# Optimization experiments

Hardware: AMD Instinct MI355X
Metric: run time of the kernel (lower is better)

Reference implementation:

```python
import jax, jax.numpy as jnp
import numpy as np

H, F, K, R = 8, 64, 10, 256  # num_heads, in_features, num_sines, num_realizations
B, L = 4, 2048


def setup_inputs() -> dict:
    key = jax.random.key(0)
    k1, k2, k3, k4, k5, k6 = jax.random.split(key, 6)
    return {
        "queries": jax.random.normal(k1, (B, L, H, F), dtype=jnp.float32),
        "keys": jax.random.normal(k2, (B, L, H, F), dtype=jnp.float32),
        "z": jax.random.normal(k3, (B, H, F, 2 * K, R), dtype=jnp.float32),
        "freqs": jax.random.normal(k4, (H, F, K), dtype=jnp.float32),
        "offsets": jax.random.normal(k5, (H, F, K), dtype=jnp.float32),
        "gains": jax.random.normal(k6, (H, F, K), dtype=jnp.float32),
    }


def reference(queries, keys, z, freqs, offsets, gains):
    h, f_dim, k_sines = freqs.shape
    length = queries.shape[1]
    r = z.shape[-1]
    # split positional / non-positional features (rest is empty here: key_dim == in_features)
    q_pos, q_rest = queries[..., :f_dim], queries[..., f_dim:]
    k_pos, k_rest = keys[..., :f_dim], keys[..., f_dim:]

    idx = jnp.arange(length, dtype=queries.dtype)  # linspace(0, L-1, L)
    fr = jax.nn.sigmoid(freqs)[:, :, None, :] / 2.0          # [H, F, 1, K]
    base = 2.0 * jnp.pi * fr * idx[None, None, :, None]       # [H, F, L, K]
    ph_q = base + offsets[:, :, None, :]
    ph_k = base
    # stack(cos, sin) on last axis then flatten -> interleaved cos0,sin0,... : [H, F, L, 2K]
    omega_q = jnp.stack([jnp.cos(ph_q), jnp.sin(ph_q)], axis=-1).reshape(h, f_dim, length, 2 * k_sines)
    omega_k = jnp.stack([jnp.cos(ph_k), jnp.sin(ph_k)], axis=-1).reshape(h, f_dim, length, 2 * k_sines)

    g = jnp.tile(jax.nn.softplus(gains), (1, 1, 2))           # [H, F, 2K] (block-repeated, as in torch .repeat)
    zs = z * g[None, :, :, :, None] / np.sqrt(r * f_dim).astype(np.float32)  # [B, H, F, 2K, R]

    # fused double contraction over f (in_features) and s (2K sines); equals
    # (omega @ z) permuted then multiplied by queries and summed over in_features
    qhat = jnp.einsum('hfls,bhfsr,blhf->blhr', omega_q, zs, q_pos)  # [B, L, H, R]
    khat = jnp.einsum('hfls,bhfsr,blhf->blhr', omega_k, zs, k_pos)

    qhat = jnp.concatenate([qhat, q_rest], axis=-1)
    khat = jnp.concatenate([khat, k_rest], axis=-1)
    return qhat, khat
```

## Files before the change

### kernel.cpp

```cpp
#include <hip/hip_runtime.h>
#include <math.h>


#define NH 8
#define NF 64
#define NK 10
#define NR 256
#define NB 4
#define NL 2048
#define KTOT 1280
#define BM 128
#define BK 32
#define NCH (KTOT/BK)
#define NFRAG_B 16
#define WS_NEEDED ((size_t)NB*NH*NCH*NFRAG_B*1024)

typedef __attribute__((ext_vector_type(8))) short short8;
typedef __attribute__((ext_vector_type(4))) float f32x4;
typedef __attribute__((ext_vector_type(4))) unsigned int u32x4;

static __device__ __forceinline__ unsigned short f2b(float f) {
    unsigned x = __float_as_uint(f);
    return (unsigned short)((x + 0x7FFFu + ((x >> 16) & 1u)) >> 16);
}
static __device__ __forceinline__ unsigned int pk2(float a, float b) {
    return (unsigned int)f2b(a) | ((unsigned int)f2b(b) << 16);
}
static __device__ __forceinline__ void gload_lds16(const void* g, void* l) {
    __builtin_amdgcn_global_load_lds(
        (const __attribute__((address_space(1))) unsigned int*)g,
        (__attribute__((address_space(3))) unsigned int*)l, 16, 0, 0);
}

__global__ __launch_bounds__(256)
void spe_prep(const float* __restrict__ z, const float* __restrict__ gains,
              unsigned char* __restrict__ bpack)
{
    __shared__ float s_g[NF*NK];
    const int ch  = blockIdx.x;
    const int bh  = blockIdx.y;
    const int h   = bh & 7;
    const int tid = threadIdx.x;
    for (int i = tid; i < NF*NK; i += 256)
        s_g[i] = log1pf(expf(gains[h*NF*NK + i])) * 0.0078125f;
    __syncthreads();
    const float* zb = z + (size_t)bh * KTOT * NR;
    unsigned char* dst = bpack + ((size_t)(bh*NCH + ch) * NFRAG_B) * 1024;
    #pragma unroll
    for (int it = 0; it < 4; ++it) {
        const int s  = tid + 256*it;
        const int fi = s >> 6;
        const int l  = s & 63;
        const int r  = fi*16 + (l & 15);
        const int k0 = ch*BK + (l >> 4)*8;
        u32x4 wv;
        #pragma unroll
        for (int jp = 0; jp < 4; ++jp) {
            const int ka = k0 + 2*jp, kb = ka + 1;
            const int fa = (ka*3277) >> 16; int sa = ka - fa*20; if (sa >= NK) sa -= NK;
            const int fb = (kb*3277) >> 16; int sb = kb - fb*20; if (sb >= NK) sb -= NK;
            const float va = zb[(size_t)ka*NR + r] * s_g[fa*NK + sa];
            const float vb = zb[(size_t)kb*NR + r] * s_g[fb*NK + sb];
            wv[jp] = pk2(va, vb);
        }
        *(u32x4*)(dst + (size_t)s*16) = wv;
    }
}

#define OFF_B0  0
#define OFF_B1  16384
#define OFF_A   32768
#define OFF_POS 40960
#define OFF_FR  57472
#define OFF_OF  60032
#define SMEM_SZ 62592

__global__ __launch_bounds__(512, 4)
void spe_main(const float* __restrict__ queries, const float* __restrict__ keys,
              const float* __restrict__ freqs, const float* __restrict__ offsets,
              const unsigned char* __restrict__ bpack, float* __restrict__ out)
{
    __shared__ __attribute__((aligned(16))) unsigned char smem[SMEM_SZ];
    const int tid  = threadIdx.x;
    const int lane = tid & 63;
    const int w    = tid >> 6;
    const int l0   = blockIdx.x * BM;
    const int bh   = blockIdx.y;
    const int b = bh >> 3, h = bh & 7;
    const int isK  = blockIdx.z;

    float* ld_fr = (float*)(smem + OFF_FR);
    float* ld_of = (float*)(smem + OFF_OF);
    unsigned short* pos_t = (unsigned short*)(smem + OFF_POS);

    for (int i = tid; i < NF*NK; i += 512) {
        const float fv = freqs[h*NF*NK + i];
        ld_fr[i] = 0.5f / (1.0f + expf(-fv));
        ld_of[i] = isK ? 0.0f : offsets[h*NF*NK + i] * 0.15915494309189535f;
    }
    {
        const float* pos = isK ? keys : queries;
        #pragma unroll
        for (int i = 0; i < 4; ++i) {
            const int lrow = (tid >> 4) + 32*i;
            const int f0   = (tid & 15) * 4;
            const float4 v = *(const float4*)(pos + ((size_t)((b*NL + l0 + lrow)*NH + h))*NF + f0);
            pos_t[(f0+0)*129 + lrow] = f2b(v.x);
            pos_t[(f0+1)*129 + lrow] = f2b(v.y);
            pos_t[(f0+2)*129 + lrow] = f2b(v.z);
            pos_t[(f0+3)*129 + lrow] = f2b(v.w);
        }
    }
    __syncthreads();

    const unsigned char* bp = bpack + (size_t)bh * ((size_t)NCH*NFRAG_B*1024);
    const int fi0 = w*2;
    gload_lds16(bp + (size_t)fi0*1024 + lane*16,       smem + OFF_B0 + (fi0  <<10));
    gload_lds16(bp + (size_t)(fi0+1)*1024 + lane*16,   smem + OFF_B0 + ((fi0+1)<<10));

    const int wm = w >> 2, wn = w & 3;
    f32x4 acc[4][4];
    #pragma unroll
    for (int mi = 0; mi < 4; ++mi)
        #pragma unroll
        for (int ni = 0; ni < 4; ++ni)
            acc[mi][ni] = (f32x4){0.f, 0.f, 0.f, 0.f};

    const int o_m = tid & 3;
    const int m_m = tid >> 2;
    const float lf = (float)(l0 + m_m);
    const int a_byte = (m_m >> 4)*1024 + (o_m*16 + (m_m & 15))*16;

    for (int t = 0; t < NCH; ++t) {
        unsigned char* Bcur = smem + ((t & 1) ? OFF_B1 : OFF_B0);
        unsigned char* Bnxt = smem + ((t & 1) ? OFF_B0 : OFF_B1);

        u32x4 wv;
        #pragma unroll
        for (int jp = 0; jp < 4; ++jp) {
            const int kk   = t*BK + o_m*8 + 2*jp;
            const int f    = (kk*3277) >> 16;
            const int srem = kk - f*20;
            const int kidx = f*NK + (srem >> 1);
            const float x  = __builtin_amdgcn_fractf(ld_of[kidx] + ld_fr[kidx]*lf);
            const float c  = __builtin_amdgcn_cosf(x);
            const float sn = __builtin_amdgcn_sinf(x);
            const float p  = __uint_as_float(((unsigned)pos_t[f*129 + m_m]) << 16);
            wv[jp] = pk2(c*p, sn*p);
        }

        asm volatile("s_waitcnt vmcnt(0)" ::: "memory");
        __builtin_amdgcn_sched_barrier(0);
        __builtin_amdgcn_s_barrier();

        if (t + 1 < NCH) {
            gload_lds16(bp + (size_t)((t+1)*NFRAG_B + fi0)*1024 + lane*16,
                        Bnxt + (fi0<<10));
            gload_lds16(bp + (size_t)((t+1)*NFRAG_B + fi0+1)*1024 + lane*16,
                        Bnxt + ((fi0+1)<<10));
        }

        *(u32x4*)(smem + OFF_A + a_byte) = wv;
        asm volatile("s_waitcnt lgkmcnt(0)" ::: "memory");
        __builtin_amdgcn_sched_barrier(0);
        __builtin_amdgcn_s_barrier();

        short8 bf[4];
        #pragma unroll
        for (int ni = 0; ni < 4; ++ni)
            bf[ni] = *(const short8*)(Bcur + ((wn*4 + ni) << 10) + (lane << 4));
        #pragma unroll
        for (int mi = 0; mi < 4; ++mi) {
            const short8 af = *(const short8*)(smem + OFF_A + ((wm*4 + mi) << 10) + (lane << 4));
            #pragma unroll
            for (int ni = 0; ni < 4; ++ni)
                acc[mi][ni] = __builtin_amdgcn_mfma_f32_16x16x32_bf16(af, bf[ni], acc[mi][ni], 0, 0, 0);
        }
    }

    const size_t qk_off = (size_t)isK * ((size_t)NB*NL*NH*NR);
    const int row_l = (lane >> 4) * 4;
    const int col_r = lane & 15;
    #pragma unroll
    for (int mi = 0; mi < 4; ++mi) {
        const int lg = l0 + wm*64 + mi*16 + row_l;
        #pragma unroll
        for (int ni = 0; ni < 4; ++ni) {
            const int rg = wn*64 + ni*16 + col_r;
            const f32x4 v = acc[mi][ni];
            #pragma unroll
            for (int q = 0; q < 4; ++q)
                out[qk_off + ((size_t)((b*NL + lg + q)*NH + h))*NR + rg] = v[q];
        }
    }
}

#define FOFF_B   0
#define FOFF_A   32768
#define FOFF_POS 49152
#define FOFF_FR  65536
#define FOFF_OFS 68096
#define FOFF_GS  70656
#define FSMEM_SZ 73216

__global__ __launch_bounds__(512, 4)
void spe_mfma_fb(const float* __restrict__ queries, const float* __restrict__ keys,
                 const float* __restrict__ z, const float* __restrict__ freqs,
                 const float* __restrict__ offsets, const float* __restrict__ gains,
                 float* __restrict__ out)
{
    __shared__ __attribute__((aligned(16))) unsigned char smem[FSMEM_SZ];
    const int tid = threadIdx.x, lane = tid & 63;
    const int l0 = blockIdx.x * BM, bh = blockIdx.y;
    const int b = bh >> 3, h = bh & 7, isK = blockIdx.z;
    float* ld_fr = (float*)(smem + FOFF_FR);
    float* ld_of = (float*)(smem + FOFF_OFS);
    float* ld_gs = (float*)(smem + FOFF_GS);
    unsigned short* pos_t = (unsigned short*)(smem + FOFF_POS);
    for (int i = tid; i < NF*NK; i += 512) {
        const float fv = freqs[h*NF*NK + i];
        ld_fr[i] = 0.5f / (1.0f + expf(-fv));
        ld_of[i] = isK ? 0.0f : offsets[h*NF*NK + i] * 0.15915494309189535f;
        ld_gs[i] = log1pf(expf(gains[h*NF*NK + i])) * 0.0078125f;
    }
    {
        const float* pos = isK ? keys : queries;
        #pragma unroll
        for (int i = 0; i < 4; ++i) {
            const int lrow = (tid >> 4) + 32*i;
            const int f0 = (tid & 15) * 4;
            const float4 v = *(const float4*)(pos + ((size_t)((b*NL + l0 + lrow)*NH + h))*NF + f0);
            pos_t[(f0+0)*BM + lrow] = f2b(v.x); pos_t[(f0+1)*BM + lrow] = f2b(v.y);
            pos_t[(f0+2)*BM + lrow] = f2b(v.z); pos_t[(f0+3)*BM + lrow] = f2b(v.w);
        }
    }
    __syncthreads();
    const int w = tid >> 6, wm = w >> 2, wn = w & 3;
    f32x4 acc[4][4];
    #pragma unroll
    for (int mi = 0; mi < 4; ++mi)
        #pragma unroll
        for (int ni = 0; ni < 4; ++ni) acc[mi][ni] = (f32x4){0.f,0.f,0.f,0.f};
    const float* zbh = z + (size_t)(b*NH + h) * ((size_t)KTOT*NR);
    for (int ch = 0; ch < KTOT/64; ++ch) {
        const int fs0 = ch * 64;
        #pragma unroll
        for (int i = 0; i < 4; ++i) {
            const int tau = tid + 512*i, r = tau & 255, krun = tau >> 8;
            const float* zp = zbh + (size_t)(fs0 + krun*8)*NR + r;
            u32x4 wv2;
            #pragma unroll
            for (int jp = 0; jp < 4; ++jp) {
                const int fs = fs0 + krun*8 + 2*jp;
                const int f = (fs*3277) >> 16; const int rem = fs - f*20;
                const int km = (rem >= NK) ? rem - NK : rem;
                const int kn = ((rem+1) >= NK && (rem+1) < 2*NK) ? rem+1-NK : rem+1;
                const float sc0 = ld_gs[f*NK + km], sc1 = ld_gs[f*NK + (kn < NK ? kn : kn-NK)];
                wv2[jp] = pk2(zp[(2*jp)*NR]*sc0, zp[(2*jp+1)*NR]*sc1);
            }
            *(u32x4*)(smem + FOFF_B + ((((krun>>2)*16) + (r>>4)) << 10)
                                    + ((((krun&3)*16) + (r&15)) << 4)) = wv2;
        }
        #pragma unroll
        for (int i = 0; i < 2; ++i) {
            const int tau = tid + 512*i, m = tau & 127, krun = tau >> 7;
            const float lff = (float)(l0 + m);
            u32x4 wv2;
            #pragma unroll
            for (int jp = 0; jp < 4; ++jp) {
                const int fs = fs0 + krun*8 + 2*jp;
                const int f = (fs*3277) >> 16; const int rem = fs - f*20;
                const int kidx = f*NK + (rem >> 1);
                const float x = __builtin_amdgcn_fractf(ld_of[kidx] + ld_fr[kidx]*lff);
                const float c = __builtin_amdgcn_cosf(x), sn = __builtin_amdgcn_sinf(x);
                const float p = __uint_as_float(((unsigned)pos_t[f*BM + m]) << 16);
                wv2[jp] = pk2(c*p, sn*p);
            }
            *(u32x4*)(smem + FOFF_A + ((((krun>>2)*8) + (m>>4)) << 10)
                                    + ((((krun&3)*16) + (m&15)) << 4)) = wv2;
        }
        __syncthreads();
        #pragma unroll
        for (int ks = 0; ks < 2; ++ks) {
            short8 bf[4];
            #pragma unroll
            for (int ni = 0; ni < 4; ++ni)
                bf[ni] = *(const short8*)(smem + FOFF_B + ((ks*16 + wn*4 + ni) << 10) + (lane << 4));
            #pragma unroll
            for (int mi = 0; mi < 4; ++mi) {
                const short8 af = *(const short8*)(smem + FOFF_A + ((ks*8 + wm*4 + mi) << 10) + (lane << 4));
                #pragma unroll
                for (int ni = 0; ni < 4; ++ni)
                    acc[mi][ni] = __builtin_amdgcn_mfma_f32_16x16x32_bf16(af, bf[ni], acc[mi][ni], 0, 0, 0);
            }
        }
        __syncthreads();
    }
    const size_t qk_off = (size_t)isK * ((size_t)NB*NL*NH*NR);
    const int row_l = (lane >> 4) * 4, col_r = lane & 15;
    #pragma unroll
    for (int mi = 0; mi < 4; ++mi) {
        const int lg = l0 + wm*64 + mi*16 + row_l;
        #pragma unroll
        for (int ni = 0; ni < 4; ++ni) {
            const int rg = wn*64 + ni*16 + col_r;
            const f32x4 v = acc[mi][ni];
            #pragma unroll
            for (int q = 0; q < 4; ++q)
                out[qk_off + ((size_t)((b*NL + lg + q)*NH + h))*NR + rg] = v[q];
        }
    }
}

extern "C" void kernel_launch(void* const* d_in, const int* in_sizes, int n_in,
                              void* d_out, int out_size, void* d_ws, size_t ws_size,
                              hipStream_t stream) {
    const float* queries = (const float*)d_in[0];
    const float* keys    = (const float*)d_in[1];
    const float* z       = (const float*)d_in[2];
    const float* freqs   = (const float*)d_in[3];
    const float* offsets = (const float*)d_in[4];
    const float* gains   = (const float*)d_in[5];
    float* out = (float*)d_out;

    if (ws_size >= WS_NEEDED) {
        unsigned char* bpack = (unsigned char*)d_ws;
        spe_prep<<<dim3(NCH, NB*NH), 256, 0, stream>>>(z, gains, bpack);
        spe_main<<<dim3(NL/BM, NB*NH, 2), 512, 0, stream>>>(queries, keys, freqs, offsets, bpack, out);
    } else {
        spe_mfma_fb<<<dim3(NL/BM, NB*NH, 2), 512, 0, stream>>>(queries, keys, z, freqs, offsets, gains, out);
    }
}
```

Measured before the change: 153.1 us.

## Software-pipeline A synthesis with MFMA and remap thread-to-row assignment

The A-tile sin/cos synthesis for chunk t+1 is now computed after the B fragments are loaded and before the MFMAs of chunk t, so trig math can overlap matrix-core work instead of sitting before the barrier. Each thread now owns one row with a wave-uniform k-octet, which makes the frequency/offset LDS reads broadcast-friendly. The transposed position staging buffer drops its +1 padding and is loaded with a new row/feature mapping. This adds register pressure from keeping the next chunk's packed values live across the MFMA loop.

```diff
diff --git a/kernel.cpp b/kernel.cpp
--- a/kernel.cpp
+++ b/kernel.cpp
@@ -71,9 +71,9 @@
 #define OFF_B1  16384
 #define OFF_A   32768
 #define OFF_POS 40960
-#define OFF_FR  57472
-#define OFF_OF  60032
-#define SMEM_SZ 62592
+#define OFF_FR  57344
+#define OFF_OF  59904
+#define SMEM_SZ 62464
 
 __global__ __launch_bounds__(512, 4)
 void spe_main(const float* __restrict__ queries, const float* __restrict__ keys,
@@ -100,15 +100,17 @@
     }
     {
         const float* pos = isK ? keys : queries;
-        #pragma unroll
-        for (int i = 0; i < 4; ++i) {
-            const int lrow = (tid >> 4) + 32*i;
-            const int f0   = (tid & 15) * 4;
-            const float4 v = *(const float4*)(pos + ((size_t)((b*NL + l0 + lrow)*NH + h))*NF + f0);
-            pos_t[(f0+0)*129 + lrow] = f2b(v.x);
-            pos_t[(f0+1)*129 + lrow] = f2b(v.y);
-            pos_t[(f0+2)*129 + lrow] = f2b(v.z);
-            pos_t[(f0+3)*129 + lrow] = f2b(v.w);
+        const int r  = tid >> 2;
+        const int f0 = (tid & 3) * 16;
+        const float* src = pos + ((size_t)((b*NL + l0 + r)*NH + h))*NF + f0;
+        #pragma unroll
+        for (int j = 0; j < 4; ++j) {
+            const float4 v = *(const float4*)(src + j*4);
+            const int f = f0 + j*4;
+            pos_t[(f+0)*BM + r] = f2b(v.x);
+            pos_t[(f+1)*BM + r] = f2b(v.y);
+            pos_t[(f+2)*BM + r] = f2b(v.z);
+            pos_t[(f+3)*BM + r] = f2b(v.w);
         }
     }
     __syncthreads();
@@ -126,28 +128,33 @@
         for (int ni = 0; ni < 4; ++ni)
             acc[mi][ni] = (f32x4){0.f, 0.f, 0.f, 0.f};
 
-    const int o_m = tid & 3;
-    const int m_m = tid >> 2;
-    const float lf = (float)(l0 + m_m);
-    const int a_byte = (m_m >> 4)*1024 + (o_m*16 + (m_m & 15))*16;
-
-    for (int t = 0; t < NCH; ++t) {
-        unsigned char* Bcur = smem + ((t & 1) ? OFF_B1 : OFF_B0);
-        unsigned char* Bnxt = smem + ((t & 1) ? OFF_B0 : OFF_B1);
-
+    const int a_oct  = w >> 1;
+    const int a_m    = ((w & 1) << 6) | lane;
+    const float lf   = (float)(l0 + a_m);
+    const int a_byte = (((w & 1)*4 + (lane >> 4)) << 10) + (a_oct << 8) + ((lane & 15) << 4);
+
+    auto synthA = [&](int t) -> u32x4 {
         u32x4 wv;
         #pragma unroll
         for (int jp = 0; jp < 4; ++jp) {
-            const int kk   = t*BK + o_m*8 + 2*jp;
+            const int kk   = t*BK + a_oct*8 + 2*jp;
             const int f    = (kk*3277) >> 16;
             const int srem = kk - f*20;
             const int kidx = f*NK + (srem >> 1);
             const float x  = __builtin_amdgcn_fractf(ld_of[kidx] + ld_fr[kidx]*lf);
             const float c  = __builtin_amdgcn_cosf(x);
             const float sn = __builtin_amdgcn_sinf(x);
-            const float p  = __uint_as_float(((unsigned)pos_t[f*129 + m_m]) << 16);
+            const float p  = __uint_as_float(((unsigned)pos_t[f*BM + a_m]) << 16);
             wv[jp] = pk2(c*p, sn*p);
         }
+        return wv;
+    };
+
+    u32x4 wv = synthA(0);
+
+    for (int t = 0; t < NCH; ++t) {
+        unsigned char* Bcur = smem + ((t & 1) ? OFF_B1 : OFF_B0);
+        unsigned char* Bnxt = smem + ((t & 1) ? OFF_B0 : OFF_B1);
 
         asm volatile("s_waitcnt vmcnt(0)" ::: "memory");
         __builtin_amdgcn_sched_barrier(0);
@@ -169,6 +176,9 @@
         #pragma unroll
         for (int ni = 0; ni < 4; ++ni)
             bf[ni] = *(const short8*)(Bcur + ((wn*4 + ni) << 10) + (lane << 4));
+
+        if (t + 1 < NCH) wv = synthA(t + 1);
+
         #pragma unroll
         for (int mi = 0; mi < 4; ++mi) {
             const short8 af = *(const short8*)(smem + OFF_A + ((wm*4 + mi) << 10) + (lane << 4));
```

Result: faster. 133.6 us (-12.7%).
